# Optimization experiments

Measured on AMD Instinct MI355X. Metric: run time of the kernel, lower is better.

Reference implementation:

```python
import jax, jax.numpy as jnp
import numpy as np

H = 128          # hid_feats
IN0, IN1 = 128, 64
OUT = 64         # out_feats
L = 3            # num_layers
N = 50000        # nodes per graph


def _rbf(x, W, b):
    # sklearn RBFSampler: z = sqrt(2/D) * cos(x @ W + b)
    return jnp.sqrt(2.0 / H) * jnp.cos(x @ W + b)


def _sage_branch(feat, src, dst, Wself, Wneigh, bias, n_nodes):
    # deg of each dst node (constant across layers)
    deg = jax.ops.segment_sum(jnp.ones_like(dst, dtype=feat.dtype), dst, n_nodes)
    denom = jnp.maximum(deg, 1.0)[:, None]
    for i in range(Wself.shape[0]):
        s = jax.ops.segment_sum(feat[src], dst, n_nodes)   # gather + scatter-add
        neigh = jnp.where(deg[:, None] > 0, s / denom, 0.0)
        feat = feat @ Wself[i] + neigh @ Wneigh[i] + bias[i]
    return feat


def setup_inputs() -> dict:
    key = jax.random.key(0)
    ks = jax.random.split(key, 20)
    gamma = 0.1
    inp = {}
    inp['feat0'] = jax.random.normal(ks[0], (N, IN0), jnp.float32)
    inp['feat1'] = jax.random.normal(ks[1], (N, IN1), jnp.float32)
    E = 800000
    inp['src0'] = jax.random.randint(ks[2], (E,), 0, N, jnp.int32)
    inp['dst0'] = jax.random.randint(ks[3], (E,), 0, N, jnp.int32)
    inp['src1'] = jax.random.randint(ks[4], (E,), 0, N, jnp.int32)
    inp['dst1'] = jax.random.randint(ks[5], (E,), 0, N, jnp.int32)
    # RBF random Fourier feature params (W ~ sqrt(2*gamma)*N(0,1), b ~ U[0,2pi))
    inp['rbf_W0'] = jnp.sqrt(2 * gamma) * jax.random.normal(ks[6], (IN0, H), jnp.float32)
    inp['rbf_b0'] = jax.random.uniform(ks[7], (H,), jnp.float32, 0.0, 2 * np.pi)
    inp['rbf_W1'] = jnp.sqrt(2 * gamma) * jax.random.normal(ks[8], (IN1, H), jnp.float32)
    inp['rbf_b1'] = jax.random.uniform(ks[9], (H,), jnp.float32, 0.0, 2 * np.pi)
    sc = 1.0 / np.sqrt(H)
    # branch 1 (g1) and branch 2 (g0) SAGEConv params, stacked over layers
    inp['Wself1'] = sc * jax.random.normal(ks[10], (L, H, H), jnp.float32)
    inp['Wneigh1'] = sc * jax.random.normal(ks[11], (L, H, H), jnp.float32)
    inp['b1'] = jnp.zeros((L, H), jnp.float32)
    inp['Wself2'] = sc * jax.random.normal(ks[12], (L, H, H), jnp.float32)
    inp['Wneigh2'] = sc * jax.random.normal(ks[13], (L, H, H), jnp.float32)
    inp['b2'] = jnp.zeros((L, H), jnp.float32)
    inp['fc1_W'] = sc * jax.random.normal(ks[14], (2 * H, H), jnp.float32)
    inp['fc1_b'] = jnp.zeros((H,), jnp.float32)
    inp['out_W'] = sc * jax.random.normal(ks[15], (H, OUT), jnp.float32)
    inp['out_b'] = jnp.zeros((OUT,), jnp.float32)
    inp['ro_W'] = (1.0 / np.sqrt(OUT)) * jax.random.normal(ks[16], (OUT, 1), jnp.float32)
    inp['ro_b'] = jnp.zeros((1,), jnp.float32)
    return inp


def reference(feat0, feat1, src0, dst0, src1, dst1,
              rbf_W0, rbf_b0, rbf_W1, rbf_b1,
              Wself1, Wneigh1, b1, Wself2, Wneigh2, b2,
              fc1_W, fc1_b, out_W, out_b, ro_W, ro_b):
    # branch 1: g1 path-complex features
    h1 = _rbf(feat1, rbf_W1, rbf_b1)
    y1 = _sage_branch(h1, src1, dst1, Wself1, Wneigh1, b1, feat1.shape[0])
    # branch 2: g0 node features
    h0 = _rbf(feat0, rbf_W0, rbf_b0)
    y2 = _sage_branch(h0, src0, dst0, Wself2, Wneigh2, b2, feat0.shape[0])
    # adaptive_avg_pool1d to 1 == mean over nodes
    y = jnp.concatenate([y2.mean(axis=0), y1.mean(axis=0)], axis=0)  # [2H]
    h = jax.nn.relu(y @ fc1_W + fc1_b)          # dropout is identity in eval
    h = jax.nn.leaky_relu(h @ out_W + out_b, negative_slope=0.01)
    return h @ ro_W + ro_b                      # [1]
```

## Files before the change

kernel.cpp:

```cpp
#include <hip/hip_runtime.h>
#include <math.h>

#define HF   128
#define CAPW 64
#define HB   64

__global__ __launch_bounds__(256) void histgemm_kernel(const float* __restrict__ A,
                                                       const float* __restrict__ W,
                                                       const float* __restrict__ bias,
                                                       float* __restrict__ hout,
                                                       float* __restrict__ partial,
                                                       const int* __restrict__ s0, const int* __restrict__ d0,
                                                       const int* __restrict__ s1, const int* __restrict__ d1,
                                                       unsigned int* __restrict__ cntbuf,
                                                       int N, int E, int histBlocks){
  __shared__ __align__(16) unsigned int sm32[12544];

  const int t = threadIdx.x;
  const int HW = (N + 3) >> 2;

  if ((int)blockIdx.x < histBlocks){
    const int bid = blockIdx.x;
    const int b  = bid & 63;
    const int br = (bid >> 6) & 1;
    const int z  = bid >> 7;
    const int* keys = z ? (br ? d1 : d0) : (br ? s1 : s0);
    for (int w = t; w < HW; w += 256) sm32[w] = 0u;
    __syncthreads();
    const int C  = (E + HB - 1) / HB;
    const int lo = b * C;
    int hi = lo + C; if (hi > E) hi = E;
    for (int i = lo + t; i < hi; i += 256){
      int k = keys[i];
      atomicAdd(&sm32[k >> 2], 1u << ((k & 3) << 3));
    }
    __syncthreads();
    unsigned int* out = cntbuf + ((size_t)(z * 2 + br) * HB + b) * HW;
    for (int w = t; w < HW; w += 256) out[w] = sm32[w];
    return;
  }

  float (*As)[68]   = (float(*)[68])sm32;
  float (*Bs)[132]  = (float(*)[132])((float*)sm32 + 1088);
  float (*red)[128] = (float(*)[128])sm32;
  const int tx = t & 15;
  const int ty = t >> 4;
  const int rb = (int)blockIdx.x - histBlocks;
  const int rowbase = rb << 6;

  float acc[4][8];
  #pragma unroll
  for (int i = 0; i < 4; ++i)
    #pragma unroll
    for (int j = 0; j < 8; ++j) acc[i][j] = 0.f;

  const int ar = t >> 2;
  const int ac = (t & 3) << 2;
  const int arow = rowbase + ar;
  const int bk0 = t >> 5;
  const int bc0 = (t & 31) << 2;

  for (int k0 = 0; k0 < 128; k0 += 16){
    __syncthreads();
    float4 av = make_float4(0.f, 0.f, 0.f, 0.f);
    if (arow < N) av = *(const float4*)&A[(size_t)arow * 128 + (k0 + ac)];
    As[ac + 0][ar] = av.x; As[ac + 1][ar] = av.y;
    As[ac + 2][ar] = av.z; As[ac + 3][ar] = av.w;
    float4 b0 = *(const float4*)&W[(size_t)(k0 + bk0) * HF + bc0];
    float4 b1 = *(const float4*)&W[(size_t)(k0 + bk0 + 8) * HF + bc0];
    *(float4*)&Bs[bk0][bc0]     = b0;
    *(float4*)&Bs[bk0 + 8][bc0] = b1;
    __syncthreads();
    #pragma unroll
    for (int kk = 0; kk < 16; ++kk){
      const float4 a  = *(const float4*)&As[kk][ty << 2];
      const float4 p0 = *(const float4*)&Bs[kk][tx << 2];
      const float4 p1 = *(const float4*)&Bs[kk][64 + (tx << 2)];
      const float aa[4] = {a.x, a.y, a.z, a.w};
      const float bb[8] = {p0.x, p0.y, p0.z, p0.w, p1.x, p1.y, p1.z, p1.w};
      #pragma unroll
      for (int i = 0; i < 4; ++i)
        #pragma unroll
        for (int j = 0; j < 8; ++j)
          acc[i][j] = fmaf(aa[i], bb[j], acc[i][j]);
    }
  }

  const float4 bia0 = *(const float4*)&bias[tx << 2];
  const float4 bia1 = *(const float4*)&bias[64 + (tx << 2)];
  const float bb0[8] = {bia0.x, bia0.y, bia0.z, bia0.w, bia1.x, bia1.y, bia1.z, bia1.w};
  float o[4][8];
  float cw[8];
  #pragma unroll
  for (int j = 0; j < 8; ++j) cw[j] = 0.f;
  #pragma unroll
  for (int i = 0; i < 4; ++i){
    int row = rowbase + (ty << 2) + i;
    bool valid = row < N;
    #pragma unroll
    for (int j = 0; j < 8; ++j){
      o[i][j] = 0.125f * cosf(acc[i][j] + bb0[j]);
      if (valid) cw[j] += o[i][j];
    }
    if (valid){
      *(float4*)&hout[(size_t)row * HF + (tx << 2)]      = make_float4(o[i][0], o[i][1], o[i][2], o[i][3]);
      *(float4*)&hout[(size_t)row * HF + 64 + (tx << 2)] = make_float4(o[i][4], o[i][5], o[i][6], o[i][7]);
    }
  }

  __syncthreads();
  #pragma unroll
  for (int j = 0; j < 4; ++j){
    red[ty][(tx << 2) + j]      = cw[j];
    red[ty][64 + (tx << 2) + j] = cw[4 + j];
  }
  __syncthreads();
  for (int off = 8; off; off >>= 1){
    if (ty < off){
      #pragma unroll
      for (int j = 0; j < 4; ++j){
        red[ty][(tx << 2) + j]      += red[ty + off][(tx << 2) + j];
        red[ty][64 + (tx << 2) + j] += red[ty + off][64 + (tx << 2) + j];
      }
    }
    __syncthreads();
  }
  if (ty == 0){
    #pragma unroll
    for (int j = 0; j < 4; ++j){
      partial[(size_t)rb * 512 + (tx << 2) + j]      = red[0][(tx << 2) + j];
      partial[(size_t)rb * 512 + 64 + (tx << 2) + j] = red[0][64 + (tx << 2) + j];
    }
  }
}

__global__ __launch_bounds__(256) void scan_kernel(unsigned int* __restrict__ cntbuf,
                                                   int* __restrict__ deg,
                                                   int* __restrict__ fill, int N){
  int k = blockIdx.x * 256 + threadIdx.x;
  if (k >= 2 * N) return;
  const int br = k >= N;
  const int kk = k - br * N;
  const int HW = (N + 3) >> 2;
  unsigned char* cb = (unsigned char*)cntbuf;
  size_t dbase = ((size_t)(2 + br) * HB) * HW * 4 + kk;
  int ds = 0;
  for (int b = 0; b < HB; ++b) ds += cb[dbase + (size_t)b * HW * 4];
  deg[k] = ds;
  size_t sbase = ((size_t)(0 + br) * HB) * HW * 4 + kk;
  int run = 0;
  for (int b = 0; b < HB; ++b){
    size_t a = sbase + (size_t)b * HW * 4;
    int c = cb[a];
    cb[a] = (unsigned char)run;
    run += c;
  }
  fill[k] = run;
}

__global__ __launch_bounds__(256) void scatter_kernel(const int* __restrict__ s0, const int* __restrict__ d0,
                                                      const int* __restrict__ s1, const int* __restrict__ d1,
                                                      const unsigned int* __restrict__ cntbuf,
                                                      unsigned short* __restrict__ slots,
                                                      int N, int E){
  __shared__ unsigned int sm32[12544];
  const int t  = threadIdx.x;
  const int b  = blockIdx.x & 63;
  const int br = blockIdx.x >> 6;
  const int HW = (N + 3) >> 2;
  const unsigned int* offw = cntbuf + ((size_t)br * HB + b) * HW;
  for (int w = t; w < HW; w += 256) sm32[w] = offw[w];
  __syncthreads();
  const int* srcA = br ? s1 : s0;
  const int* dstA = br ? d1 : d0;
  const int C  = (E + HB - 1) / HB;
  const int lo = b * C;
  int hi = lo + C; if (hi > E) hi = E;
  const size_t obase = (size_t)br * N;
  for (int i = lo + t; i < hi; i += 256){
    int s = srcA[i];
    int d = dstA[i];
    unsigned int old = atomicAdd(&sm32[s >> 2], 1u << ((s & 3) << 3));
    int j = (old >> ((s & 3) << 3)) & 0xff;
    if (j < CAPW) slots[(obase + s) * CAPW + j] = (unsigned short)d;
  }
}

__global__ __launch_bounds__(256) void pull1_kernel(const unsigned short* __restrict__ slots,
                                                    const int* __restrict__ fill,
                                                    const int* __restrict__ deg,
                                                    float* __restrict__ w1,
                                                    float* __restrict__ qa,
                                                    double* __restrict__ S, int N){
  int i = blockIdx.x * 256 + threadIdx.x;
  int t = threadIdx.x;
  float a = 0.f;
  int dgi = 0;
  int br = 0;
  bool valid = i < 2 * N;
  if (valid){
    br = i >= N;
    int o = br * N;
    int c = fill[i]; if (c > CAPW) c = CAPW;
    const unsigned short* sl = slots + (size_t)i * CAPW;
    int j = 0;
    for (; j + 3 < c; j += 4){
      int dA = sl[j], dB = sl[j+1], dC = sl[j+2], dD = sl[j+3];
      a += 1.f/(float)deg[o+dA] + 1.f/(float)deg[o+dB]
         + 1.f/(float)deg[o+dC] + 1.f/(float)deg[o+dD];
    }
    for (; j < c; ++j) a += 1.f/(float)deg[o + sl[j]];
    dgi = deg[i];
    w1[i] = a;
    qa[i] = dgi > 0 ? a * (1.f/(float)dgi) : 0.f;
  }
  __shared__ double rd[4][256];
  bool pos = valid && dgi > 0;
  rd[0][t] = (pos && !br) ? 1.0 : 0.0;
  rd[1][t] = (pos && !br) ? (double)a : 0.0;
  rd[2][t] = (pos &&  br) ? 1.0 : 0.0;
  rd[3][t] = (pos &&  br) ? (double)a : 0.0;
  __syncthreads();
  for (int off = 128; off; off >>= 1){
    if (t < off){
      rd[0][t] += rd[0][t+off]; rd[1][t] += rd[1][t+off];
      rd[2][t] += rd[2][t+off]; rd[3][t] += rd[3][t+off];
    }
    __syncthreads();
  }
  if (t < 4) atomicAdd(&S[t], rd[t][0]);
}

template<bool WQ>
__global__ __launch_bounds__(256) void pull_kernel(const unsigned short* __restrict__ slots,
                                                   const int* __restrict__ fill,
                                                   const int* __restrict__ deg,
                                                   const float* __restrict__ qin,
                                                   float* __restrict__ wout,
                                                   float* __restrict__ qout, int N){
  int i = blockIdx.x * 256 + threadIdx.x;
  if (i >= 2 * N) return;
  int br = i >= N;
  int o = br * N;
  int c = fill[i]; if (c > CAPW) c = CAPW;
  const unsigned short* sl = slots + (size_t)i * CAPW;
  float a = 0.f;
  int j = 0;
  for (; j + 3 < c; j += 4){
    int dA = sl[j], dB = sl[j+1], dC = sl[j+2], dD = sl[j+3];
    a += qin[o+dA] + qin[o+dB] + qin[o+dC] + qin[o+dD];
  }
  for (; j < c; ++j) a += qin[o + sl[j]];
  wout[i] = a;
  if (WQ){
    int dgi = deg[i];
    qout[i] = dgi > 0 ? a * (1.f/(float)dgi) : 0.f;
  }
}

__global__ __launch_bounds__(256) void tail_kernel(const float* __restrict__ A1,
                                                   const float* __restrict__ W1,
                                                   const float* __restrict__ bias1,
                                                   const float* __restrict__ h0,
                                                   const float* __restrict__ w1,
                                                   const float* __restrict__ w2,
                                                   const float* __restrict__ w3,
                                                   float* __restrict__ partial0,
                                                   float* __restrict__ partial1,
                                                   int N, int gg){
  __shared__ __align__(16) float smem[3200];
  float (*As)[68]   = (float(*)[68])smem;
  float (*Bs)[132]  = (float(*)[132])(smem + 1088);
  float (*red)[128] = (float(*)[128])smem;
  const int t  = threadIdx.x;
  const int tx = t & 15;
  const int ty = t >> 4;

  if ((int)blockIdx.x >= gg){
    const int wb = blockIdx.x - gg;
    const int rowbase = wb << 6;
    float o[4][8];
    float wr[3][4];
    #pragma unroll
    for (int i = 0; i < 4; ++i){
      int row = rowbase + (ty << 2) + i;
      bool valid = row < N;
      float4 x0 = make_float4(0,0,0,0), x1 = make_float4(0,0,0,0);
      if (valid){
        x0 = *(const float4*)&h0[(size_t)row * HF + (tx << 2)];
        x1 = *(const float4*)&h0[(size_t)row * HF + 64 + (tx << 2)];
      }
      o[i][0]=x0.x; o[i][1]=x0.y; o[i][2]=x0.z; o[i][3]=x0.w;
      o[i][4]=x1.x; o[i][5]=x1.y; o[i][6]=x1.z; o[i][7]=x1.w;
      wr[0][i] = valid ? w1[row] : 0.f;
      wr[1][i] = valid ? w2[row] : 0.f;
      wr[2][i] = valid ? w3[row] : 0.f;
    }
    #pragma unroll
    for (int k = 0; k < 3; ++k){
      float cw[8];
      #pragma unroll
      for (int j = 0; j < 8; ++j)
        cw[j] = wr[k][0]*o[0][j] + wr[k][1]*o[1][j] + wr[k][2]*o[2][j] + wr[k][3]*o[3][j];
      __syncthreads();
      #pragma unroll
      for (int j = 0; j < 4; ++j){
        red[ty][(tx << 2) + j]      = cw[j];
        red[ty][64 + (tx << 2) + j] = cw[4 + j];
      }
      __syncthreads();
      for (int off = 8; off; off >>= 1){
        if (ty < off){
          #pragma unroll
          for (int j = 0; j < 4; ++j){
            red[ty][(tx << 2) + j]      += red[ty + off][(tx << 2) + j];
            red[ty][64 + (tx << 2) + j] += red[ty + off][64 + (tx << 2) + j];
          }
        }
        __syncthreads();
      }
      if (ty == 0){
        #pragma unroll
        for (int j = 0; j < 4; ++j){
          partial0[(size_t)wb * 512 + (k + 1) * 128 + (tx << 2) + j]      = red[0][(tx << 2) + j];
          partial0[(size_t)wb * 512 + (k + 1) * 128 + 64 + (tx << 2) + j] = red[0][64 + (tx << 2) + j];
        }
      }
      __syncthreads();
    }
    return;
  }

  const int rowbase = (int)blockIdx.x << 6;
  float acc[4][8];
  #pragma unroll
  for (int i = 0; i < 4; ++i)
    #pragma unroll
    for (int j = 0; j < 8; ++j) acc[i][j] = 0.f;

  const int ar = t >> 2;
  const int ac = (t & 3) << 2;
  const int arow = rowbase + ar;
  const int bk0 = t >> 5;
  const int bc0 = (t & 31) << 2;

  for (int k0 = 0; k0 < 64; k0 += 16){
    __syncthreads();
    float4 av = make_float4(0.f, 0.f, 0.f, 0.f);
    if (arow < N) av = *(const float4*)&A1[(size_t)arow * 64 + (k0 + ac)];
    As[ac + 0][ar] = av.x; As[ac + 1][ar] = av.y;
    As[ac + 2][ar] = av.z; As[ac + 3][ar] = av.w;
    float4 b0 = *(const float4*)&W1[(size_t)(k0 + bk0) * HF + bc0];
    float4 b1 = *(const float4*)&W1[(size_t)(k0 + bk0 + 8) * HF + bc0];
    *(float4*)&Bs[bk0][bc0]     = b0;
    *(float4*)&Bs[bk0 + 8][bc0] = b1;
    __syncthreads();
    #pragma unroll
    for (int kk = 0; kk < 16; ++kk){
      const float4 a  = *(const float4*)&As[kk][ty << 2];
      const float4 p0 = *(const float4*)&Bs[kk][tx << 2];
      const float4 p1 = *(const float4*)&Bs[kk][64 + (tx << 2)];
      const float aa[4] = {a.x, a.y, a.z, a.w};
      const float bb[8] = {p0.x, p0.y, p0.z, p0.w, p1.x, p1.y, p1.z, p1.w};
      #pragma unroll
      for (int i = 0; i < 4; ++i)
        #pragma unroll
        for (int j = 0; j < 8; ++j)
          acc[i][j] = fmaf(aa[i], bb[j], acc[i][j]);
    }
  }

  const float4 bia0 = *(const float4*)&bias1[tx << 2];
  const float4 bia1 = *(const float4*)&bias1[64 + (tx << 2)];
  const float bb0[8] = {bia0.x, bia0.y, bia0.z, bia0.w, bia1.x, bia1.y, bia1.z, bia1.w};
  float o[4][8];
  float wr[4][4];
  #pragma unroll
  for (int i = 0; i < 4; ++i){
    int row = rowbase + (ty << 2) + i;
    bool valid = row < N;
    #pragma unroll
    for (int j = 0; j < 8; ++j)
      o[i][j] = 0.125f * cosf(acc[i][j] + bb0[j]);
    wr[0][i] = valid ? 1.f : 0.f;
    wr[1][i] = valid ? w1[N + row] : 0.f;
    wr[2][i] = valid ? w2[N + row] : 0.f;
    wr[3][i] = valid ? w3[N + row] : 0.f;
  }
  __syncthreads();
  #pragma unroll
  for (int k = 0; k < 4; ++k){
    float cw[8];
    #pragma unroll
    for (int j = 0; j < 8; ++j)
      cw[j] = wr[k][0]*o[0][j] + wr[k][1]*o[1][j] + wr[k][2]*o[2][j] + wr[k][3]*o[3][j];
    #pragma unroll
    for (int j = 0; j < 4; ++j){
      red[ty][(tx << 2) + j]      = cw[j];
      red[ty][64 + (tx << 2) + j] = cw[4 + j];
    }
    __syncthreads();
    for (int off = 8; off; off >>= 1){
      if (ty < off){
        #pragma unroll
        for (int j = 0; j < 4; ++j){
          red[ty][(tx << 2) + j]      += red[ty + off][(tx << 2) + j];
          red[ty][64 + (tx << 2) + j] += red[ty + off][64 + (tx << 2) + j];
        }
      }
      __syncthreads();
    }
    if (ty == 0){
      #pragma unroll
      for (int j = 0; j < 4; ++j){
        partial1[(size_t)blockIdx.x * 512 + k * 128 + (tx << 2) + j]      = red[0][(tx << 2) + j];
        partial1[(size_t)blockIdx.x * 512 + k * 128 + 64 + (tx << 2) + j] = red[0][64 + (tx << 2) + j];
      }
    }
    __syncthreads();
  }
}

__global__ __launch_bounds__(512) void greduce_kernel(const float* __restrict__ partial,
                                                      double* __restrict__ G, int nb, int stride){
  int br = blockIdx.y;
  const float* p = partial + (size_t)br * stride;
  double* Gb = G + 512 * br;
  int t = threadIdx.x;
  double s = 0.0;
  for (int b = blockIdx.x; b < nb; b += gridDim.x) s += (double)p[(size_t)b * 512 + t];
  atomicAdd(&Gb[t], s);
}

__global__ __launch_bounds__(512) void head_kernel(const double* __restrict__ G,
                                                   const double* __restrict__ S,
                                                   const float* __restrict__ WsA, const float* __restrict__ WnA, const float* __restrict__ bA,
                                                   const float* __restrict__ WsB, const float* __restrict__ WnB, const float* __restrict__ bB,
                                                   float* __restrict__ ymean, int n){
  const int br = blockIdx.x;
  const double* Gb = G + 512 * br;
  const double* Sb = S + 2 * br;
  const float* Ws   = br ? WsB : WsA;
  const float* Wn   = br ? WnB : WnA;
  const float* bias = br ? bB  : bA;
  float* yout = ymean + 128 * br;

  __shared__ double g[4][128], ng[3][128];
  __shared__ float lws[32][128], lwn[32][128];
  const int t = threadIdx.x;
  const int k = t >> 7, j = t & 127;
  g[k][j] = Gb[t];
  double s[4];
  s[0] = (double)n; s[1] = Sb[0]; s[2] = Sb[1]; s[3] = 0.0;

  for (int i = 0; i < 3; ++i){
    const float* ws = Ws + (size_t)i * 16384;
    const float* wn = Wn + (size_t)i * 16384;
    const float* bi = bias + (size_t)i * 128;
    const int kmax = 2 - i;
    double a = (k <= kmax) ? s[k] * (double)bi[j] : 0.0;
    for (int mc = 0; mc < 128; mc += 32){
      __syncthreads();
      #pragma unroll
      for (int p = 0; p < 2; ++p){
        int idx = (p * 512 + t) << 2;
        int mm = idx >> 7, cc = idx & 127;
        *(float4*)&lws[mm][cc] = *(const float4*)&ws[(size_t)(mc + mm) * 128 + cc];
        *(float4*)&lwn[mm][cc] = *(const float4*)&wn[(size_t)(mc + mm) * 128 + cc];
      }
      __syncthreads();
      if (k <= kmax){
        #pragma unroll
        for (int m = 0; m < 32; ++m){
          a += g[k][mc + m]     * (double)lws[m][j];
          a += g[k + 1][mc + m] * (double)lwn[m][j];
        }
      }
    }
    __syncthreads();
    if (k <= kmax) ng[k][j] = a;
    __syncthreads();
    if (k <= kmax) g[k][j] = ng[k][j];
  }
  __syncthreads();
  if (t < 128) yout[t] = (float)(g[0][t] / (double)n);
}

__global__ void final_kernel(const float* __restrict__ ymean,
                             const float* __restrict__ fc1W, const float* __restrict__ fc1b,
                             const float* __restrict__ outW, const float* __restrict__ outb,
                             const float* __restrict__ roW, const float* __restrict__ rob,
                             float* __restrict__ out){
  __shared__ float y[256], h1[128], h2[64];
  int t = threadIdx.x;
  y[t] = ymean[t];
  __syncthreads();
  if (t < 128){
    float a = fc1b[t];
    for (int k = 0; k < 256; ++k) a = fmaf(y[k], fc1W[k * 128 + t], a);
    h1[t] = a > 0.f ? a : 0.f;
  }
  __syncthreads();
  if (t < 64){
    float a = outb[t];
    for (int k = 0; k < 128; ++k) a = fmaf(h1[k], outW[k * 64 + t], a);
    h2[t] = a > 0.f ? a : 0.01f * a;
  }
  __syncthreads();
  if (t == 0){
    float a = rob[0];
    for (int k = 0; k < 64; ++k) a = fmaf(h2[k], roW[k], a);
    out[0] = a;
  }
}

extern "C" void kernel_launch(void* const* d_in, const int* in_sizes, int n_in,
                              void* d_out, int out_size, void* d_ws, size_t ws_size,
                              hipStream_t stream){
  const float* feat0  = (const float*)d_in[0];
  const float* feat1  = (const float*)d_in[1];
  const int*   src0   = (const int*)d_in[2];
  const int*   dst0   = (const int*)d_in[3];
  const int*   src1   = (const int*)d_in[4];
  const int*   dst1   = (const int*)d_in[5];
  const float* rbfW0  = (const float*)d_in[6];
  const float* rbfb0  = (const float*)d_in[7];
  const float* rbfW1  = (const float*)d_in[8];
  const float* rbfb1  = (const float*)d_in[9];
  const float* Wself1 = (const float*)d_in[10];
  const float* Wneigh1= (const float*)d_in[11];
  const float* b1     = (const float*)d_in[12];
  const float* Wself2 = (const float*)d_in[13];
  const float* Wneigh2= (const float*)d_in[14];
  const float* b2     = (const float*)d_in[15];
  const float* fc1W   = (const float*)d_in[16];
  const float* fc1b   = (const float*)d_in[17];
  const float* outW   = (const float*)d_in[18];
  const float* outb   = (const float*)d_in[19];
  const float* roW    = (const float*)d_in[20];
  const float* rob    = (const float*)d_in[21];

  const int N = in_sizes[0] / 128;
  const int E = in_sizes[2];
  const int HW = (N + 3) >> 2;

  char* w = (char*)d_ws;
  size_t off = 0;
  auto alloc = [&](size_t bytes) -> char* {
    char* p = w + off; off += (bytes + 255) & ~(size_t)255; return p;
  };
  int*    deg    = (int*)   alloc((size_t)2 * N * 4);
  int*    fill   = (int*)   alloc((size_t)2 * N * 4);
  float*  w1     = (float*) alloc((size_t)2 * N * 4);
  float*  w2     = (float*) alloc((size_t)2 * N * 4);
  float*  w3     = (float*) alloc((size_t)2 * N * 4);
  float*  qa     = (float*) alloc((size_t)2 * N * 4);
  float*  qb     = (float*) alloc((size_t)2 * N * 4);
  double* S      = (double*)alloc(4 * sizeof(double));
  double* G      = (double*)alloc(1024 * sizeof(double));
  float*  ymean  = (float*) alloc(256 * sizeof(float));
  const int gg   = (N + 63) >> 6;
  float*  partial= (float*) alloc((size_t)2 * gg * 512 * 4);
  float*  h0buf  = (float*) alloc((size_t)N * HF * 4);
  unsigned short* slots = (unsigned short*)alloc((size_t)2 * N * CAPW * 2);
  unsigned int* cntbuf  = (unsigned int*)alloc((size_t)4 * HB * HW * 4);

  const size_t slen = (size_t)((char*)ymean - (char*)S);

  const int nGrid2 = (2 * N + 255) >> 8;

  hipMemsetAsync(S, 0, slen, stream);
  histgemm_kernel<<<256 + gg, 256, 0, stream>>>(feat0, rbfW0, rbfb0, h0buf, partial,
                                                src0, dst0, src1, dst1, cntbuf, N, E, 256);
  scan_kernel<<<nGrid2, 256, 0, stream>>>(cntbuf, deg, fill, N);
  scatter_kernel<<<128, 256, 0, stream>>>(src0, dst0, src1, dst1, cntbuf, slots, N, E);
  pull1_kernel<<<nGrid2, 256, 0, stream>>>(slots, fill, deg, w1, qa, S, N);
  pull_kernel<true ><<<nGrid2, 256, 0, stream>>>(slots, fill, deg, qa, w2, qb, N);
  pull_kernel<false><<<nGrid2, 256, 0, stream>>>(slots, fill, deg, qb, w3, qb, N);
  tail_kernel<<<2 * gg, 256, 0, stream>>>(feat1, rbfW1, rbfb1, h0buf, w1, w2, w3,
                                          partial, partial + (size_t)gg * 512, N, gg);
  greduce_kernel<<<dim3(16, 2), 512, 0, stream>>>(partial, G, gg, gg * 512);
  head_kernel<<<2, 512, 0, stream>>>(G, S, Wself2, Wneigh2, b2, Wself1, Wneigh1, b1, ymean, N);
  final_kernel<<<1, 256, 0, stream>>>(ymean, fc1W, fc1b, outW, outb, roW, rob, (float*)d_out);
}
```

Before: 216.1 us.

## Recompute branch-0 RBF GEMM in tail instead of storing h0 buffer

```diff
diff --git a/kernel.cpp b/kernel.cpp
--- a/kernel.cpp
+++ b/kernel.cpp
@@ -5,133 +5,29 @@
 #define CAPW 64
 #define HB   64
 
-__global__ __launch_bounds__(256) void histgemm_kernel(const float* __restrict__ A,
-                                                       const float* __restrict__ W,
-                                                       const float* __restrict__ bias,
-                                                       float* __restrict__ hout,
-                                                       float* __restrict__ partial,
-                                                       const int* __restrict__ s0, const int* __restrict__ d0,
-                                                       const int* __restrict__ s1, const int* __restrict__ d1,
-                                                       unsigned int* __restrict__ cntbuf,
-                                                       int N, int E, int histBlocks){
-  __shared__ __align__(16) unsigned int sm32[12544];
-
+__global__ __launch_bounds__(256) void hist_kernel(const int* __restrict__ s0, const int* __restrict__ d0,
+                                                   const int* __restrict__ s1, const int* __restrict__ d1,
+                                                   unsigned int* __restrict__ cntbuf,
+                                                   int N, int E){
+  __shared__ unsigned int sm32[12544];
   const int t = threadIdx.x;
   const int HW = (N + 3) >> 2;
-
-  if ((int)blockIdx.x < histBlocks){
-    const int bid = blockIdx.x;
-    const int b  = bid & 63;
-    const int br = (bid >> 6) & 1;
-    const int z  = bid >> 7;
-    const int* keys = z ? (br ? d1 : d0) : (br ? s1 : s0);
-    for (int w = t; w < HW; w += 256) sm32[w] = 0u;
-    __syncthreads();
-    const int C  = (E + HB - 1) / HB;
-    const int lo = b * C;
-    int hi = lo + C; if (hi > E) hi = E;
-    for (int i = lo + t; i < hi; i += 256){
-      int k = keys[i];
-      atomicAdd(&sm32[k >> 2], 1u << ((k & 3) << 3));
-    }
-    __syncthreads();
-    unsigned int* out = cntbuf + ((size_t)(z * 2 + br) * HB + b) * HW;
-    for (int w = t; w < HW; w += 256) out[w] = sm32[w];
-    return;
-  }
-
-  float (*As)[68]   = (float(*)[68])sm32;
-  float (*Bs)[132]  = (float(*)[132])((float*)sm32 + 1088);
-  float (*red)[128] = (float(*)[128])sm32;
-  const int tx = t & 15;
-  const int ty = t >> 4;
-  const int rb = (int)blockIdx.x - histBlocks;
-  const int rowbase = rb << 6;
-
-  float acc[4][8];
-  #pragma unroll
-  for (int i = 0; i < 4; ++i)
-    #pragma unroll
-    for (int j = 0; j < 8; ++j) acc[i][j] = 0.f;
-
-  const int ar = t >> 2;
-  const int ac = (t & 3) << 2;
-  const int arow = rowbase + ar;
-  const int bk0 = t >> 5;
-  const int bc0 = (t & 31) << 2;
-
-  for (int k0 = 0; k0 < 128; k0 += 16){
-    __syncthreads();
-    float4 av = make_float4(0.f, 0.f, 0.f, 0.f);
-    if (arow < N) av = *(const float4*)&A[(size_t)arow * 128 + (k0 + ac)];
-    As[ac + 0][ar] = av.x; As[ac + 1][ar] = av.y;
-    As[ac + 2][ar] = av.z; As[ac + 3][ar] = av.w;
-    float4 b0 = *(const float4*)&W[(size_t)(k0 + bk0) * HF + bc0];
-    float4 b1 = *(const float4*)&W[(size_t)(k0 + bk0 + 8) * HF + bc0];
-    *(float4*)&Bs[bk0][bc0]     = b0;
-    *(float4*)&Bs[bk0 + 8][bc0] = b1;
-    __syncthreads();
-    #pragma unroll
-    for (int kk = 0; kk < 16; ++kk){
-      const float4 a  = *(const float4*)&As[kk][ty << 2];
-      const float4 p0 = *(const float4*)&Bs[kk][tx << 2];
-      const float4 p1 = *(const float4*)&Bs[kk][64 + (tx << 2)];
-      const float aa[4] = {a.x, a.y, a.z, a.w};
-      const float bb[8] = {p0.x, p0.y, p0.z, p0.w, p1.x, p1.y, p1.z, p1.w};
-      #pragma unroll
-      for (int i = 0; i < 4; ++i)
-        #pragma unroll
-        for (int j = 0; j < 8; ++j)
-          acc[i][j] = fmaf(aa[i], bb[j], acc[i][j]);
-    }
-  }
-
-  const float4 bia0 = *(const float4*)&bias[tx << 2];
-  const float4 bia1 = *(const float4*)&bias[64 + (tx << 2)];
-  const float bb0[8] = {bia0.x, bia0.y, bia0.z, bia0.w, bia1.x, bia1.y, bia1.z, bia1.w};
-  float o[4][8];
-  float cw[8];
-  #pragma unroll
-  for (int j = 0; j < 8; ++j) cw[j] = 0.f;
-  #pragma unroll
-  for (int i = 0; i < 4; ++i){
-    int row = rowbase + (ty << 2) + i;
-    bool valid = row < N;
-    #pragma unroll
-    for (int j = 0; j < 8; ++j){
-      o[i][j] = 0.125f * cosf(acc[i][j] + bb0[j]);
-      if (valid) cw[j] += o[i][j];
-    }
-    if (valid){
-      *(float4*)&hout[(size_t)row * HF + (tx << 2)]      = make_float4(o[i][0], o[i][1], o[i][2], o[i][3]);
-      *(float4*)&hout[(size_t)row * HF + 64 + (tx << 2)] = make_float4(o[i][4], o[i][5], o[i][6], o[i][7]);
-    }
-  }
-
-  __syncthreads();
-  #pragma unroll
-  for (int j = 0; j < 4; ++j){
-    red[ty][(tx << 2) + j]      = cw[j];
-    red[ty][64 + (tx << 2) + j] = cw[4 + j];
-  }
-  __syncthreads();
-  for (int off = 8; off; off >>= 1){
-    if (ty < off){
-      #pragma unroll
-      for (int j = 0; j < 4; ++j){
-        red[ty][(tx << 2) + j]      += red[ty + off][(tx << 2) + j];
-        red[ty][64 + (tx << 2) + j] += red[ty + off][64 + (tx << 2) + j];
-      }
-    }
-    __syncthreads();
-  }
-  if (ty == 0){
-    #pragma unroll
-    for (int j = 0; j < 4; ++j){
-      partial[(size_t)rb * 512 + (tx << 2) + j]      = red[0][(tx << 2) + j];
-      partial[(size_t)rb * 512 + 64 + (tx << 2) + j] = red[0][64 + (tx << 2) + j];
-    }
-  }
+  const int b  = blockIdx.x & 63;
+  const int br = (blockIdx.x >> 6) & 1;
+  const int z  = blockIdx.x >> 7;
+  const int* keys = z ? (br ? d1 : d0) : (br ? s1 : s0);
+  for (int w = t; w < HW; w += 256) sm32[w] = 0u;
+  __syncthreads();
+  const int C  = (E + HB - 1) / HB;
+  const int lo = b * C;
+  int hi = lo + C; if (hi > E) hi = E;
+  for (int i = lo + t; i < hi; i += 256){
+    int k = keys[i];
+    atomicAdd(&sm32[k >> 2], 1u << ((k & 3) << 3));
+  }
+  __syncthreads();
+  unsigned int* out = cntbuf + ((size_t)(z * 2 + br) * HB + b) * HW;
+  for (int w = t; w < HW; w += 256) out[w] = sm32[w];
 }
 
 __global__ __launch_bounds__(256) void scan_kernel(unsigned int* __restrict__ cntbuf,
@@ -204,10 +100,13 @@
     int c = fill[i]; if (c > CAPW) c = CAPW;
     const unsigned short* sl = slots + (size_t)i * CAPW;
     int j = 0;
-    for (; j + 3 < c; j += 4){
+    for (; j + 7 < c; j += 8){
       int dA = sl[j], dB = sl[j+1], dC = sl[j+2], dD = sl[j+3];
+      int dE = sl[j+4], dF = sl[j+5], dG = sl[j+6], dH = sl[j+7];
       a += 1.f/(float)deg[o+dA] + 1.f/(float)deg[o+dB]
-         + 1.f/(float)deg[o+dC] + 1.f/(float)deg[o+dD];
+         + 1.f/(float)deg[o+dC] + 1.f/(float)deg[o+dD]
+         + 1.f/(float)deg[o+dE] + 1.f/(float)deg[o+dF]
+         + 1.f/(float)deg[o+dG] + 1.f/(float)deg[o+dH];
     }
     for (; j < c; ++j) a += 1.f/(float)deg[o + sl[j]];
     dgi = deg[i];
@@ -246,9 +145,11 @@
   const unsigned short* sl = slots + (size_t)i * CAPW;
   float a = 0.f;
   int j = 0;
-  for (; j + 3 < c; j += 4){
+  for (; j + 7 < c; j += 8){
     int dA = sl[j], dB = sl[j+1], dC = sl[j+2], dD = sl[j+3];
-    a += qin[o+dA] + qin[o+dB] + qin[o+dC] + qin[o+dD];
+    int dE = sl[j+4], dF = sl[j+5], dG = sl[j+6], dH = sl[j+7];
+    a += qin[o+dA] + qin[o+dB] + qin[o+dC] + qin[o+dD]
+       + qin[o+dE] + qin[o+dF] + qin[o+dG] + qin[o+dH];
   }
   for (; j < c; ++j) a += qin[o + sl[j]];
   wout[i] = a;
@@ -258,80 +159,21 @@
   }
 }
 
-__global__ __launch_bounds__(256) void tail_kernel(const float* __restrict__ A1,
-                                                   const float* __restrict__ W1,
-                                                   const float* __restrict__ bias1,
-                                                   const float* __restrict__ h0,
-                                                   const float* __restrict__ w1,
-                                                   const float* __restrict__ w2,
-                                                   const float* __restrict__ w3,
-                                                   float* __restrict__ partial0,
-                                                   float* __restrict__ partial1,
-                                                   int N, int gg){
-  __shared__ __align__(16) float smem[3200];
-  float (*As)[68]   = (float(*)[68])smem;
-  float (*Bs)[132]  = (float(*)[132])(smem + 1088);
-  float (*red)[128] = (float(*)[128])smem;
+template<int K1>
+__device__ __forceinline__ void gemmred_body(const float* __restrict__ A,
+                                             const float* __restrict__ W,
+                                             const float* __restrict__ bias,
+                                             const float* __restrict__ w1,
+                                             const float* __restrict__ w2,
+                                             const float* __restrict__ w3,
+                                             int wo, float* __restrict__ partial,
+                                             int rb, int N,
+                                             float (*As)[68], float (*Bs)[132], float (*red)[128]){
   const int t  = threadIdx.x;
   const int tx = t & 15;
   const int ty = t >> 4;
-
-  if ((int)blockIdx.x >= gg){
-    const int wb = blockIdx.x - gg;
-    const int rowbase = wb << 6;
-    float o[4][8];
-    float wr[3][4];
-    #pragma unroll
-    for (int i = 0; i < 4; ++i){
-      int row = rowbase + (ty << 2) + i;
-      bool valid = row < N;
-      float4 x0 = make_float4(0,0,0,0), x1 = make_float4(0,0,0,0);
-      if (valid){
-        x0 = *(const float4*)&h0[(size_t)row * HF + (tx << 2)];
-        x1 = *(const float4*)&h0[(size_t)row * HF + 64 + (tx << 2)];
-      }
-      o[i][0]=x0.x; o[i][1]=x0.y; o[i][2]=x0.z; o[i][3]=x0.w;
-      o[i][4]=x1.x; o[i][5]=x1.y; o[i][6]=x1.z; o[i][7]=x1.w;
-      wr[0][i] = valid ? w1[row] : 0.f;
-      wr[1][i] = valid ? w2[row] : 0.f;
-      wr[2][i] = valid ? w3[row] : 0.f;
-    }
-    #pragma unroll
-    for (int k = 0; k < 3; ++k){
-      float cw[8];
-      #pragma unroll
-      for (int j = 0; j < 8; ++j)
-        cw[j] = wr[k][0]*o[0][j] + wr[k][1]*o[1][j] + wr[k][2]*o[2][j] + wr[k][3]*o[3][j];
-      __syncthreads();
-      #pragma unroll
-      for (int j = 0; j < 4; ++j){
-        red[ty][(tx << 2) + j]      = cw[j];
-        red[ty][64 + (tx << 2) + j] = cw[4 + j];
-      }
-      __syncthreads();
-      for (int off = 8; off; off >>= 1){
-        if (ty < off){
-          #pragma unroll
-          for (int j = 0; j < 4; ++j){
-            red[ty][(tx << 2) + j]      += red[ty + off][(tx << 2) + j];
-            red[ty][64 + (tx << 2) + j] += red[ty + off][64 + (tx << 2) + j];
-          }
-        }
-        __syncthreads();
-      }
-      if (ty == 0){
-        #pragma unroll
-        for (int j = 0; j < 4; ++j){
-          partial0[(size_t)wb * 512 + (k + 1) * 128 + (tx << 2) + j]      = red[0][(tx << 2) + j];
-          partial0[(size_t)wb * 512 + (k + 1) * 128 + 64 + (tx << 2) + j] = red[0][64 + (tx << 2) + j];
-        }
-      }
-      __syncthreads();
-    }
-    return;
-  }
-
-  const int rowbase = (int)blockIdx.x << 6;
+  const int rowbase = rb << 6;
+
   float acc[4][8];
   #pragma unroll
   for (int i = 0; i < 4; ++i)
@@ -344,14 +186,14 @@
   const int bk0 = t >> 5;
   const int bc0 = (t & 31) << 2;
 
-  for (int k0 = 0; k0 < 64; k0 += 16){
+  for (int k0 = 0; k0 < K1; k0 += 16){
     __syncthreads();
     float4 av = make_float4(0.f, 0.f, 0.f, 0.f);
-    if (arow < N) av = *(const float4*)&A1[(size_t)arow * 64 + (k0 + ac)];
+    if (arow < N) av = *(const float4*)&A[(size_t)arow * K1 + (k0 + ac)];
     As[ac + 0][ar] = av.x; As[ac + 1][ar] = av.y;
     As[ac + 2][ar] = av.z; As[ac + 3][ar] = av.w;
-    float4 b0 = *(const float4*)&W1[(size_t)(k0 + bk0) * HF + bc0];
-    float4 b1 = *(const float4*)&W1[(size_t)(k0 + bk0 + 8) * HF + bc0];
+    float4 b0 = *(const float4*)&W[(size_t)(k0 + bk0) * HF + bc0];
+    float4 b1 = *(const float4*)&W[(size_t)(k0 + bk0 + 8) * HF + bc0];
     *(float4*)&Bs[bk0][bc0]     = b0;
     *(float4*)&Bs[bk0 + 8][bc0] = b1;
     __syncthreads();
@@ -370,8 +212,8 @@
     }
   }
 
-  const float4 bia0 = *(const float4*)&bias1[tx << 2];
-  const float4 bia1 = *(const float4*)&bias1[64 + (tx << 2)];
+  const float4 bia0 = *(const float4*)&bias[tx << 2];
+  const float4 bia1 = *(const float4*)&bias[64 + (tx << 2)];
   const float bb0[8] = {bia0.x, bia0.y, bia0.z, bia0.w, bia1.x, bia1.y, bia1.z, bia1.w};
   float o[4][8];
   float wr[4][4];
@@ -383,9 +225,9 @@
     for (int j = 0; j < 8; ++j)
       o[i][j] = 0.125f * cosf(acc[i][j] + bb0[j]);
     wr[0][i] = valid ? 1.f : 0.f;
-    wr[1][i] = valid ? w1[N + row] : 0.f;
-    wr[2][i] = valid ? w2[N + row] : 0.f;
-    wr[3][i] = valid ? w3[N + row] : 0.f;
+    wr[1][i] = valid ? w1[wo + row] : 0.f;
+    wr[2][i] = valid ? w2[wo + row] : 0.f;
+    wr[3][i] = valid ? w3[wo + row] : 0.f;
   }
   __syncthreads();
   #pragma unroll
@@ -413,12 +255,34 @@
     if (ty == 0){
       #pragma unroll
       for (int j = 0; j < 4; ++j){
-        partial1[(size_t)blockIdx.x * 512 + k * 128 + (tx << 2) + j]      = red[0][(tx << 2) + j];
-        partial1[(size_t)blockIdx.x * 512 + k * 128 + 64 + (tx << 2) + j] = red[0][64 + (tx << 2) + j];
+        partial[(size_t)rb * 512 + k * 128 + (tx << 2) + j]      = red[0][(tx << 2) + j];
+        partial[(size_t)rb * 512 + k * 128 + 64 + (tx << 2) + j] = red[0][64 + (tx << 2) + j];
       }
     }
     __syncthreads();
   }
+}
+
+__global__ __launch_bounds__(256) void gemmred2_kernel(const float* __restrict__ A0,
+                                                       const float* __restrict__ W0,
+                                                       const float* __restrict__ b0,
+                                                       const float* __restrict__ A1,
+                                                       const float* __restrict__ W1,
+                                                       const float* __restrict__ b1,
+                                                       const float* __restrict__ w1,
+                                                       const float* __restrict__ w2,
+                                                       const float* __restrict__ w3,
+                                                       float* __restrict__ partial,
+                                                       int N, int gg){
+  __shared__ __align__(16) float smem[3200];
+  float (*As)[68]   = (float(*)[68])smem;
+  float (*Bs)[132]  = (float(*)[132])(smem + 1088);
+  float (*red)[128] = (float(*)[128])smem;
+  if ((int)blockIdx.x < gg)
+    gemmred_body<128>(A0, W0, b0, w1, w2, w3, 0, partial, blockIdx.x, N, As, Bs, red);
+  else
+    gemmred_body<64>(A1, W1, b1, w1, w2, w3, N, partial + (size_t)gg * 512,
+                     blockIdx.x - gg, N, As, Bs, red);
 }
 
 __global__ __launch_bounds__(512) void greduce_kernel(const float* __restrict__ partial,
@@ -462,8 +326,8 @@
     for (int mc = 0; mc < 128; mc += 32){
       __syncthreads();
       #pragma unroll
-      for (int p = 0; p < 2; ++p){
-        int idx = (p * 512 + t) << 2;
+      for (int pp = 0; pp < 2; ++pp){
+        int idx = (pp * 512 + t) << 2;
         int mm = idx >> 7, cc = idx & 127;
         *(float4*)&lws[mm][cc] = *(const float4*)&ws[(size_t)(mc + mm) * 128 + cc];
         *(float4*)&lwn[mm][cc] = *(const float4*)&wn[(size_t)(mc + mm) * 128 + cc];
@@ -561,7 +425,6 @@
   float*  ymean  = (float*) alloc(256 * sizeof(float));
   const int gg   = (N + 63) >> 6;
   float*  partial= (float*) alloc((size_t)2 * gg * 512 * 4);
-  float*  h0buf  = (float*) alloc((size_t)N * HF * 4);
   unsigned short* slots = (unsigned short*)alloc((size_t)2 * N * CAPW * 2);
   unsigned int* cntbuf  = (unsigned int*)alloc((size_t)4 * HB * HW * 4);
 
@@ -570,15 +433,14 @@
   const int nGrid2 = (2 * N + 255) >> 8;
 
   hipMemsetAsync(S, 0, slen, stream);
-  histgemm_kernel<<<256 + gg, 256, 0, stream>>>(feat0, rbfW0, rbfb0, h0buf, partial,
-                                                src0, dst0, src1, dst1, cntbuf, N, E, 256);
+  hist_kernel<<<256, 256, 0, stream>>>(src0, dst0, src1, dst1, cntbuf, N, E);
   scan_kernel<<<nGrid2, 256, 0, stream>>>(cntbuf, deg, fill, N);
   scatter_kernel<<<128, 256, 0, stream>>>(src0, dst0, src1, dst1, cntbuf, slots, N, E);
   pull1_kernel<<<nGrid2, 256, 0, stream>>>(slots, fill, deg, w1, qa, S, N);
   pull_kernel<true ><<<nGrid2, 256, 0, stream>>>(slots, fill, deg, qa, w2, qb, N);
   pull_kernel<false><<<nGrid2, 256, 0, stream>>>(slots, fill, deg, qb, w3, qb, N);
-  tail_kernel<<<2 * gg, 256, 0, stream>>>(feat1, rbfW1, rbfb1, h0buf, w1, w2, w3,
-                                          partial, partial + (size_t)gg * 512, N, gg);
+  gemmred2_kernel<<<2 * gg, 256, 0, stream>>>(feat0, rbfW0, rbfb0, feat1, rbfW1, rbfb1,
+                                              w1, w2, w3, partial, N, gg);
   greduce_kernel<<<dim3(16, 2), 512, 0, stream>>>(partial, G, gg, gg * 512);
   head_kernel<<<2, 512, 0, stream>>>(G, S, Wself2, Wneigh2, b2, Wself1, Wneigh1, b1, ymean, N);
   final_kernel<<<1, 256, 0, stream>>>(ymean, fc1W, fc1b, outW, outb, roW, rob, (float*)d_out);
```

After: 216.2 us. About the same (+0.1%).
